# Kernel tuning notes

Hardware: AMD Instinct MI355X
Metric: run time of the kernel (lower is better)

The kernel has to match this reference:

```python
import jax, jax.numpy as jnp
import numpy as np

L, H, M, KB = 8, 512, 32, 256  # layers, hidden, fourier modes, key bits
EPS = 1e-5


def setup_inputs() -> dict:
    key = jax.random.key(0)
    ks = jax.random.split(key, 20)
    B, S = 8, 2048
    s = 0.02
    return {
        'x': jax.random.normal(ks[0], (B, S), jnp.float32),
        # input projection Linear(1, H): weight [H] (squeezed), bias [H]
        'in_w': jax.random.normal(ks[1], (H,), jnp.float32) * s,
        'in_b': jax.random.normal(ks[2], (H,), jnp.float32) * s,
        # per-layer fourier weights (complex, stored as real/imag), conv1d(k=1), layernorm
        'fw_r': jax.random.normal(ks[3], (L, M, H, H), jnp.float32) * s,
        'fw_i': jax.random.normal(ks[4], (L, M, H, H), jnp.float32) * s,
        'conv_w': jax.random.normal(ks[5], (L, H, H), jnp.float32) / np.sqrt(H),
        'conv_b': jax.random.normal(ks[6], (L, H), jnp.float32) * s,
        'ln_g': jnp.ones((L, H), jnp.float32),
        'ln_b': jnp.zeros((L, H), jnp.float32),
        # output projection H -> H/2 -> H/4 -> 1
        'op1_w': jax.random.normal(ks[7], (H // 2, H), jnp.float32) / np.sqrt(H),
        'op1_b': jnp.zeros((H // 2,), jnp.float32),
        'op2_w': jax.random.normal(ks[8], (H // 4, H // 2), jnp.float32) / np.sqrt(H // 2),
        'op2_b': jnp.zeros((H // 4,), jnp.float32),
        'op3_w': jax.random.normal(ks[9], (1, H // 4), jnp.float32) / np.sqrt(H // 4),
        'op3_b': jnp.zeros((1,), jnp.float32),
        # cryptanalytic head H -> H -> KB (sigmoid)
        'h1_w': jax.random.normal(ks[10], (H, H), jnp.float32) / np.sqrt(H),
        'h1_b': jnp.zeros((H,), jnp.float32),
        'h2_w': jax.random.normal(ks[11], (KB, H), jnp.float32) / np.sqrt(H),
        'h2_b': jnp.zeros((KB,), jnp.float32),
    }


def _gelu(x):
    return jax.nn.gelu(x, approximate=False)


def _fourier_layer(x, Wc, cw, cb, g, b):
    # x: [B, S, H]; Wc: [M, H, H] complex
    S = x.shape[1]
    x_ft = jnp.fft.rfft(x, axis=1)  # [B, F, H] complex, F = S//2+1
    m = min(M, x_ft.shape[1])
    # batched per-mode complex GEMM (replaces python loop over modes)
    spec = jnp.einsum('bmh,mhk->bmk', x_ft[:, :m], Wc[:m])
    out_ft = jnp.concatenate([spec, jnp.zeros_like(x_ft[:, m:])], axis=1)
    x_fourier = jnp.fft.irfft(out_ft, n=S, axis=1)  # real [B, S, H]
    x_conv = x @ cw.T + cb  # Conv1d kernel-size-1 == per-position linear
    y = x_fourier + x_conv
    mu = jnp.mean(y, axis=-1, keepdims=True)
    var = jnp.var(y, axis=-1, keepdims=True)
    return (y - mu) * jax.lax.rsqrt(var + EPS) * g + b


def reference(x, in_w, in_b, fw_r, fw_i, conv_w, conv_b, ln_g, ln_b,
              op1_w, op1_b, op2_w, op2_b, op3_w, op3_b,
              h1_w, h1_b, h2_w, h2_b):
    # input projection: Linear(1, H) on x[..., None]
    h = x[:, :, None] * in_w[None, None, :] + in_b  # [B, S, H]
    Wc = fw_r + 1j * fw_i  # [L, M, H, H]
    for l in range(L):
        h = _fourier_layer(h, Wc[l], conv_w[l], conv_b[l], ln_g[l], ln_b[l]) + h
    # output projection (dropout is identity in eval)
    o = _gelu(h @ op1_w.T + op1_b)
    o = _gelu(o @ op2_w.T + op2_b)
    output = (o @ op3_w.T + op3_b)[..., 0]  # [B, S]
    gf = jnp.mean(h, axis=1)  # [B, H]
    k = _gelu(gf @ h1_w.T + h1_b)
    key_pred = jax.nn.sigmoid(k @ h2_w.T + h2_b)  # [B, KB]
    return output, key_pred
```

## Files before the change

kernel.cpp:

```cpp
#include <hip/hip_runtime.h>
#include <hip/hip_bf16.h>
#include <math.h>

#define BB   8
#define SEQ  2048
#define HD   512
#define LAY  8
#define MD   32
#define NKB  256
#define LNEPS 1e-5f

typedef __attribute__((ext_vector_type(8))) short v8s;
typedef __attribute__((ext_vector_type(4))) float v4f;
typedef __attribute__((ext_vector_type(4))) unsigned short v4us;

__device__ __forceinline__ float b2f(__hip_bfloat16 v) { return __bfloat162float(v); }
__device__ __forceinline__ float geluf(float v) { return v * 0.5f * (1.f + erff(v * 0.70710678118654752f)); }
__device__ __forceinline__ float bflo(unsigned int u) { return __uint_as_float((u & 0xFFFFu) << 16); }
__device__ __forceinline__ float bfhi(unsigned int u) { return __uint_as_float(u & 0xFFFF0000u); }

__device__ __forceinline__ float ldin(const void* p, size_t i, int bf) {
    if (bf) return __bfloat162float(((const __hip_bfloat16*)p)[i]);
    return ((const float*)p)[i];
}
__device__ __forceinline__ void stout(void* p, size_t i, float v, int bf) {
    if (bf) ((__hip_bfloat16*)p)[i] = __float2bfloat16(v);
    else    ((float*)p)[i] = v;
}

__device__ __forceinline__ void gl2lds16(const void* g, void* l) {
    __builtin_amdgcn_global_load_lds((__attribute__((address_space(1))) void*)g,
                                     (__attribute__((address_space(3))) void*)l, 16, 0, 0);
}

__device__ __forceinline__ unsigned short f2bfu(float f) {
    __hip_bfloat16 b = __float2bfloat16(f);
    return *(unsigned short*)&b;
}

__global__ void k_flag(const unsigned int* __restrict__ lng_bits, int* __restrict__ flag) {
    if (threadIdx.x == 0 && blockIdx.x == 0)
        *flag = (lng_bits[0] == 0x3F803F80u) ? 1 : 0;
}

__global__ void k_setup(const void* __restrict__ x, const void* __restrict__ in_w, const void* __restrict__ in_b,
                        const void* __restrict__ cw, const void* __restrict__ w1, const void* __restrict__ w2,
                        const void* __restrict__ h1w, const void* __restrict__ h2w,
                        __hip_bfloat16* __restrict__ Ffwd, __hip_bfloat16* __restrict__ T2,
                        __hip_bfloat16* __restrict__ cwbf, __hip_bfloat16* __restrict__ w1bf,
                        __hip_bfloat16* __restrict__ w2bf, float* __restrict__ h1T, float* __restrict__ h2T,
                        float* __restrict__ h,
                        float* __restrict__ gf,
                        const int* __restrict__ flag) {
    int bf = *flag;
    int blk = blockIdx.x, t = threadIdx.x;
    if (blk < 512) {
        int idx = blk * 256 + t;
        int j = idx >> 11, s = idx & 2047;
        int m = j >> 1;
        int phase = (m * s) & (SEQ - 1);
        float ang = (float)phase * (6.283185307179586f / (float)SEQ);
        Ffwd[idx] = __float2bfloat16((j & 1) ? -sinf(ang) : cosf(ang));
    } else if (blk < 1024) {
        int idx = (blk - 512) * 256 + t;
        int s = idx >> 6, j = idx & 63;
        int m = j >> 1;
        float v;
        if (j == 0)      v = 1.f / (float)SEQ;
        else if (j == 1) v = 0.f;
        else {
            int phase = (m * s) & (SEQ - 1);
            float ang = (float)phase * (6.283185307179586f / (float)SEQ);
            v = (j & 1) ? (-2.f / (float)SEQ) * sinf(ang) : (2.f / (float)SEQ) * cosf(ang);
        }
        T2[idx] = __float2bfloat16(v);
    } else if (blk < 9216) {
        int idx = (blk - 1024) * 256 + t;
        cwbf[idx] = __float2bfloat16(ldin(cw, idx, bf));
    } else if (blk < 9728) {
        int idx = (blk - 9216) * 256 + t;
        w1bf[idx] = __float2bfloat16(ldin(w1, idx, bf));
    } else if (blk < 9856) {
        int idx = (blk - 9728) * 256 + t;
        w2bf[idx] = __float2bfloat16(ldin(w2, idx, bf));
    } else if (blk < 10880) {
        int idx = (blk - 9856) * 256 + t;
        int r = idx & 511, c = idx >> 9;
        h1T[idx] = ldin(h1w, (size_t)r * 512 + c, bf);
    } else if (blk < 11392) {
        int idx = (blk - 10880) * 256 + t;
        int r = idx & 255, c = idx >> 8;
        h2T[idx] = ldin(h2w, (size_t)r * 512 + c, bf);
    } else if (blk < 11408) {
        int idx = (blk - 11392) * 256 + t;
        gf[idx] = 0.f;
    } else {
        int idx = (blk - 11408) * 256 + t;
        int j = idx & 511;
        int bs = idx >> 9;
        float v = ldin(x, bs, bf) * ldin(in_w, j, bf) + ldin(in_b, j, bf);
        h[idx] = v;
    }
}

__global__ __launch_bounds__(256) void k_fdft2(const float* __restrict__ h,
                                               const __hip_bfloat16* __restrict__ Ffwd,
                                               float* __restrict__ Xpart) {
    __shared__ __align__(16) __hip_bfloat16 Als[2][16 * 72];
    int t = threadIdx.x;
    int lane = t & 63, wv = t >> 6;
    int ln15 = lane & 15, quad = lane >> 4;
    int ht = blockIdx.x, b = blockIdx.y, kh = blockIdx.z;
    int kcs = kh * 16;
    int sr = t >> 2, hc = (t & 3) * 4;

    v4f acc = (v4f){0.f, 0.f, 0.f, 0.f};

    const float* asrc0 = h + (size_t)b * SEQ * HD + ht * 16;
    const __hip_bfloat16* fbase = Ffwd + (size_t)(wv * 16 + ln15) * SEQ + quad * 8;

    float4 cur = *(const float4*)(asrc0 + (size_t)(kcs * 64 + sr) * HD + hc);
    {
        const float* cf = (const float*)&cur;
#pragma unroll
        for (int e = 0; e < 4; e++)
            Als[0][(hc + e) * 72 + sr] = __float2bfloat16(cf[e]);
    }
    __syncthreads();
    for (int i = 0; i < 16; i++) {
        int buf = i & 1;
        float4 nxt = cur;
        if (i < 15)
            nxt = *(const float4*)(asrc0 + (size_t)((kcs + i + 1) * 64 + sr) * HD + hc);
        v8s bf0 = *(const v8s*)(fbase + (kcs + i) * 64);
        v8s bf1 = *(const v8s*)(fbase + (kcs + i) * 64 + 32);
        v8s af0 = *(const v8s*)&Als[buf][ln15 * 72 + quad * 8];
        v8s af1 = *(const v8s*)&Als[buf][ln15 * 72 + 32 + quad * 8];
        acc = __builtin_amdgcn_mfma_f32_16x16x32_bf16(af0, bf0, acc, 0, 0, 0);
        acc = __builtin_amdgcn_mfma_f32_16x16x32_bf16(af1, bf1, acc, 0, 0, 0);
        if (i < 15) {
            const float* nf = (const float*)&nxt;
#pragma unroll
            for (int e = 0; e < 4; e++)
                Als[buf ^ 1][(hc + e) * 72 + sr] = __float2bfloat16(nf[e]);
        }
        __syncthreads();
        cur = nxt;
    }
    int j = wv * 16 + ln15;
    int m = j >> 1, c = j & 1;
    int hg = ht * 16 + quad * 4;
    float* outp = Xpart + (size_t)kh * 262144 + (size_t)(b * 32 + m) * 1024;
#pragma unroll
    for (int r = 0; r < 4; r++)
        outp[(size_t)(hg + r) * 2 + c] = acc[r];
}

__global__ __launch_bounds__(512) void k_mixp(const float* __restrict__ Xp0, const float* __restrict__ Xp1,
                                              const void* __restrict__ fwr, const void* __restrict__ fwi,
                                              float* __restrict__ Ppart, int l,
                                              const int* __restrict__ flag) {
    int bf = *flag;
    int ht = blockIdx.x;
    int m  = blockIdx.y;
    int t  = threadIdx.x;
    __shared__ float xs[8192];
    for (int e = t; e < 8192; e += 512) {
        int bb = e >> 10, r = e & 1023;
        size_t off = (size_t)(bb * 32 + m) * 1024 + r;
        xs[e] = Xp0[off] + Xp1[off];
    }
    __syncthreads();
    float ar[8], ai[8];
#pragma unroll
    for (int bb = 0; bb < 8; bb++) { ar[bb] = 0.f; ai[bb] = 0.f; }
    size_t wbase = (size_t)(l * 32 + m) * 262144;
    const float2* xs2 = (const float2*)xs;
    int h0 = ht * 32;
    if (bf) {
        const __hip_bfloat16* fr = (const __hip_bfloat16*)fwr;
        const __hip_bfloat16* fi = (const __hip_bfloat16*)fwi;
#pragma unroll 4
        for (int hh = h0; hh < h0 + 32; hh++) {
            float wr = b2f(fr[wbase + (size_t)hh * 512 + t]);
            float wi = b2f(fi[wbase + (size_t)hh * 512 + t]);
#pragma unroll
            for (int bb = 0; bb < 8; bb++) {
                float2 x2 = xs2[bb * 512 + hh];
                ar[bb] += x2.x * wr - x2.y * wi;
                ai[bb] += x2.x * wi + x2.y * wr;
            }
        }
    } else {
        const float* fr = (const float*)fwr;
        const float* fi = (const float*)fwi;
#pragma unroll 4
        for (int hh = h0; hh < h0 + 32; hh++) {
            float wr = fr[wbase + (size_t)hh * 512 + t];
            float wi = fi[wbase + (size_t)hh * 512 + t];
#pragma unroll
            for (int bb = 0; bb < 8; bb++) {
                float2 x2 = xs2[bb * 512 + hh];
                ar[bb] += x2.x * wr - x2.y * wi;
                ai[bb] += x2.x * wi + x2.y * wr;
            }
        }
    }
    float2* pp = (float2*)Ppart;
#pragma unroll
    for (int bb = 0; bb < 8; bb++)
        pp[((size_t)(m * 16 + ht) * 8 + bb) * 512 + t] = (float2){ar[bb], ai[bb]};
}

__global__ __launch_bounds__(256) void k_mixr(const float* __restrict__ Ppart,
                                              __hip_bfloat16* __restrict__ spec2) {
    int g = blockIdx.x * 256 + threadIdx.x;
    int k = g & 511, b = (g >> 9) & 7, m = g >> 12;
    const float2* pp = (const float2*)Ppart;
    float sr = 0.f, si = 0.f;
#pragma unroll
    for (int ht = 0; ht < 16; ht++) {
        float2 v = pp[((size_t)(m * 16 + ht) * 8 + b) * 512 + k];
        sr += v.x; si += v.y;
    }
    size_t o = ((size_t)(b * 512 + k) << 6) + 2 * m;
    __hip_bfloat16 hr = __float2bfloat16(sr), hi = __float2bfloat16(si);
    unsigned int pk = (unsigned int)*(unsigned short*)&hr | ((unsigned int)*(unsigned short*)&hi << 16);
    *(unsigned int*)(spec2 + o) = pk;
}

__global__ __launch_bounds__(512) void k_gln(__hip_bfloat16* __restrict__ hbf,
                                             const __hip_bfloat16* __restrict__ cwbf,
                                             const __hip_bfloat16* __restrict__ T2,
                                             const __hip_bfloat16* __restrict__ spec2,
                                             const void* __restrict__ cb,
                                             const void* __restrict__ lng, const void* __restrict__ lnb,
                                             float* __restrict__ h,
                                             int l, const int* __restrict__ flag) {
    int bfv = *flag;
    __shared__ __align__(16) __hip_bfloat16 smem[2][19456];
    __shared__ float stats[128];
    __hip_bfloat16* Yls = &smem[0][0];

    int t = threadIdx.x;
    int lane = t & 63, wv = t >> 6;
    int wr = wv >> 2, wc = wv & 3;
    int ln15 = lane & 15, quad = lane >> 4;
    int row0 = blockIdx.x * 64;
    int b = row0 >> 11, s0 = row0 & 2047;
    int arow = t >> 3, acolq = (t & 7) * 4;

    v4f acc[16];
#pragma unroll
    for (int i = 0; i < 16; i++) acc[i] = (v4f){0.f, 0.f, 0.f, 0.f};

    const __hip_bfloat16* cwl = cwbf + (size_t)l * 262144;

    auto stageB = [&](int buf, int kc) {
        int k0 = kc * 32;
#pragma unroll
        for (int p = 0; p < 4; p++) {
            int i = p * 512 + t;
            int n = i >> 2, kq = (i & 3) * 8;
            const __hip_bfloat16* bsrc = (k0 < 512)
                ? cwl + (size_t)n * 512 + k0 + kq
                : spec2 + (size_t)(b * 512 + n) * 64 + (k0 - 512) + kq;
            gl2lds16(bsrc, &smem[buf][2560 + (size_t)(p * 512 + wv * 64) * 8]);
        }
    };
    auto loadA = [&](int kc, float4& av, v4us& tv) {
        int k0 = kc * 32;
        if (k0 < 512) {
            av = *(const float4*)&h[(size_t)(row0 + arow) * HD + k0 + acolq];
        } else {
            tv = *(const v4us*)&T2[(size_t)(s0 + arow) * 64 + (k0 - 512) + acolq];
        }
    };
    auto writeA = [&](int buf, int kc, const float4& av, const v4us& tv) {
        __hip_bfloat16* dst = &smem[buf][arow * 40 + acolq];
        if (kc * 32 < 512) {
            const float* af = (const float*)&av;
            v4us pk;
#pragma unroll
            for (int e = 0; e < 4; e++) pk[e] = (short)f2bfu(af[e]);
            *(v4us*)dst = pk;
        } else {
            *(v4us*)dst = tv;
        }
    };

    {
        float4 av; v4us tv;
        loadA(0, av, tv);
        stageB(0, 0);
        writeA(0, 0, av, tv);
    }
    __syncthreads();
    int cur = 0;
    float4 avn; v4us tvn;
    for (int kc = 0; kc < 18; kc++) {
        if (kc < 17) {
            loadA(kc + 1, avn, tvn);
            stageB(cur ^ 1, kc + 1);
        }
        const __hip_bfloat16* Als = &smem[cur][0];
        const __hip_bfloat16* Bls = &smem[cur][2560];
        v8s af[2], bfr[8];
#pragma unroll
        for (int i = 0; i < 2; i++)
            af[i] = *(const v8s*)&Als[(wr * 32 + i * 16 + ln15) * 40 + quad * 8];
#pragma unroll
        for (int j = 0; j < 8; j++)
            bfr[j] = *(const v8s*)&Bls[(wc * 128 + j * 16 + ln15) * 32 + quad * 8];
#pragma unroll
        for (int i = 0; i < 2; i++)
#pragma unroll
            for (int j = 0; j < 8; j++)
                acc[i * 8 + j] = __builtin_amdgcn_mfma_f32_16x16x32_bf16(af[i], bfr[j], acc[i * 8 + j], 0, 0, 0);
        if (kc < 17) writeA(cur ^ 1, kc + 1, avn, tvn);
        __syncthreads();
        cur ^= 1;
    }
#pragma unroll
    for (int j = 0; j < 8; j++) {
        int col = wc * 128 + j * 16 + ln15;
        float cbv = ldin(cb, l * HD + col, bfv);
#pragma unroll
        for (int i = 0; i < 2; i++) {
            int rl = wr * 32 + i * 16 + quad * 4;
#pragma unroll
            for (int r = 0; r < 4; r++)
                Yls[(rl + r) * 520 + col] = __float2bfloat16(acc[i * 8 + j][r] + cbv);
        }
    }
    __syncthreads();
    {
        int r = t >> 3, g2 = t & 7;
        float s = 0.f, q = 0.f;
        for (int i = 0; i < 32; i++) {
            int cp = g2 + i * 8;
            unsigned int u = *(const unsigned int*)&Yls[r * 520 + cp * 2];
            float v0 = bflo(u), v1 = bfhi(u);
            s += v0 + v1; q += v0 * v0 + v1 * v1;
        }
        s += __shfl_xor(s, 1); s += __shfl_xor(s, 2); s += __shfl_xor(s, 4);
        q += __shfl_xor(q, 1); q += __shfl_xor(q, 2); q += __shfl_xor(q, 4);
        if (g2 == 0) {
            float mu = s * (1.f / (float)HD);
            float var = q * (1.f / (float)HD) - mu * mu;
            stats[r * 2] = mu; stats[r * 2 + 1] = rsqrtf(var + LNEPS);
        }
    }
    __syncthreads();
    {
        int c2 = t & 255;
        int gc = 2 * c2;
        float g0 = ldin(lng, l * HD + gc, bfv),     g1 = ldin(lng, l * HD + gc + 1, bfv);
        float b0 = ldin(lnb, l * HD + gc, bfv),     b1 = ldin(lnb, l * HD + gc + 1, bfv);
        int rbase = t >> 8;
        int last = (l == LAY - 1);
        for (int k = 0; k < 32; k++) {
            int r = rbase + 2 * k;
            float mu = stats[r * 2], rs = stats[r * 2 + 1];
            unsigned int u = *(const unsigned int*)&Yls[r * 520 + c2 * 2];
            float v0 = bflo(u), v1 = bfhi(u);
            float2 hv = *(const float2*)&h[(size_t)(row0 + r) * HD + gc];
            float n0 = (v0 - mu) * rs * g0 + b0 + hv.x;
            float n1 = (v1 - mu) * rs * g1 + b1 + hv.y;
            *(float2*)&h[(size_t)(row0 + r) * HD + gc] = (float2){n0, n1};
            if (last) {
                unsigned int up = ((unsigned int)f2bfu(n1) << 16) | (unsigned int)f2bfu(n0);
                ((unsigned int*)(hbf + (size_t)(row0 + r) * HD))[c2] = up;
            }
        }
    }
}

__global__ __launch_bounds__(256) void k_pj1(const __hip_bfloat16* __restrict__ hbf,
                                             const __hip_bfloat16* __restrict__ w1bf,
                                             const void* __restrict__ b1,
                                             __hip_bfloat16* __restrict__ o1bf,
                                             const int* __restrict__ flag) {
    int bfv = *flag;
    __shared__ __align__(16) __hip_bfloat16 smem[2][8192];
    int t = threadIdx.x;
    int lane = t & 63, wv = t >> 6;
    int wr = wv >> 1, wc = wv & 1;
    int ln15 = lane & 15, quad = lane >> 4;
    int row0 = blockIdx.x * 128, n0 = blockIdx.y * 128;

    v4f acc[16];
#pragma unroll
    for (int i = 0; i < 16; i++) acc[i] = (v4f){0.f, 0.f, 0.f, 0.f};

    auto stage = [&](int buf, int kc) {
        int k0 = kc * 32;
#pragma unroll
        for (int p = 0; p < 2; p++) {
            int i = p * 256 + t;
            int row = i >> 2, kq = (i & 3) * 8;
            gl2lds16(hbf + (size_t)(row0 + row) * 512 + k0 + kq, &smem[buf][(size_t)(p * 256 + wv * 64) * 8]);
            gl2lds16(w1bf + (size_t)(n0 + row) * 512 + k0 + kq, &smem[buf][4096 + (size_t)(p * 256 + wv * 64) * 8]);
        }
    };

    stage(0, 0);
    __syncthreads();
    int cur = 0;
    for (int kc = 0; kc < 16; kc++) {
        if (kc < 15) stage(cur ^ 1, kc + 1);
        const __hip_bfloat16* Als = &smem[cur][0];
        const __hip_bfloat16* Bls = &smem[cur][4096];
        v8s af[4], bfr[4];
#pragma unroll
        for (int i = 0; i < 4; i++)
            af[i] = *(const v8s*)&Als[(wr * 64 + i * 16 + ln15) * 32 + quad * 8];
#pragma unroll
        for (int j = 0; j < 4; j++)
            bfr[j] = *(const v8s*)&Bls[(wc * 64 + j * 16 + ln15) * 32 + quad * 8];
#pragma unroll
        for (int i = 0; i < 4; i++)
#pragma unroll
            for (int j = 0; j < 4; j++)
                acc[i * 4 + j] = __builtin_amdgcn_mfma_f32_16x16x32_bf16(af[i], bfr[j], acc[i * 4 + j], 0, 0, 0);
        __syncthreads();
        cur ^= 1;
    }
#pragma unroll
    for (int j = 0; j < 4; j++) {
        int col = n0 + wc * 64 + j * 16 + ln15;
        float bv = ldin(b1, col, bfv);
#pragma unroll
        for (int i = 0; i < 4; i++) {
            int rg = row0 + wr * 64 + i * 16 + quad * 4;
#pragma unroll
            for (int r = 0; r < 4; r++)
                o1bf[(size_t)(rg + r) * 256 + col] = __float2bfloat16(geluf(acc[i * 4 + j][r] + bv));
        }
    }
}

__global__ __launch_bounds__(256) void k_pj2(const __hip_bfloat16* __restrict__ o1bf,
                                             const __hip_bfloat16* __restrict__ w2bf,
                                             const void* __restrict__ b2,
                                             const void* __restrict__ w3, const void* __restrict__ b3,
                                             void* __restrict__ out, const int* __restrict__ flag) {
    int bfv = *flag;
    __shared__ __align__(16) __hip_bfloat16 smem[2][8192];
    __shared__ __hip_bfloat16 o2s[128 * 130];
    __shared__ float w3s[128];
    int t = threadIdx.x;
    int lane = t & 63, wv = t >> 6;
    int wr = wv >> 1, wc = wv & 1;
    int ln15 = lane & 15, quad = lane >> 4;
    int row0 = blockIdx.x * 128;
    if (t < 128) w3s[t] = ldin(w3, t, bfv);

    v4f acc[16];
#pragma unroll
    for (int i = 0; i < 16; i++) acc[i] = (v4f){0.f, 0.f, 0.f, 0.f};

    auto stage = [&](int buf, int kc) {
        int k0 = kc * 32;
#pragma unroll
        for (int p = 0; p < 2; p++) {
            int i = p * 256 + t;
            int row = i >> 2, kq = (i & 3) * 8;
            gl2lds16(o1bf + (size_t)(row0 + row) * 256 + k0 + kq, &smem[buf][(size_t)(p * 256 + wv * 64) * 8]);
            gl2lds16(w2bf + (size_t)row * 256 + k0 + kq,          &smem[buf][4096 + (size_t)(p * 256 + wv * 64) * 8]);
        }
    };

    stage(0, 0);
    __syncthreads();
    int cur = 0;
    for (int kc = 0; kc < 8; kc++) {
        if (kc < 7) stage(cur ^ 1, kc + 1);
        const __hip_bfloat16* Als = &smem[cur][0];
        const __hip_bfloat16* Bls = &smem[cur][4096];
        v8s af[4], bfr[4];
#pragma unroll
        for (int i = 0; i < 4; i++)
            af[i] = *(const v8s*)&Als[(wr * 64 + i * 16 + ln15) * 32 + quad * 8];
#pragma unroll
        for (int j = 0; j < 4; j++)
            bfr[j] = *(const v8s*)&Bls[(wc * 64 + j * 16 + ln15) * 32 + quad * 8];
#pragma unroll
        for (int i = 0; i < 4; i++)
#pragma unroll
            for (int j = 0; j < 4; j++)
                acc[i * 4 + j] = __builtin_amdgcn_mfma_f32_16x16x32_bf16(af[i], bfr[j], acc[i * 4 + j], 0, 0, 0);
        __syncthreads();
        cur ^= 1;
    }
#pragma unroll
    for (int j = 0; j < 4; j++) {
        int col = wc * 64 + j * 16 + ln15;
        float bv = ldin(b2, col, bfv);
#pragma unroll
        for (int i = 0; i < 4; i++) {
            int rl = wr * 64 + i * 16 + quad * 4;
#pragma unroll
            for (int r = 0; r < 4; r++)
                o2s[(rl + r) * 130 + col] = __float2bfloat16(geluf(acc[i * 4 + j][r] + bv));
        }
    }
    __syncthreads();
    if (t < 128) {
        float s = 0.f;
        for (int j = 0; j < 128; j++) s += b2f(o2s[t * 130 + j]) * w3s[j];
        stout(out, row0 + t, s + ldin(b3, 0, bfv), bfv);
    }
}

__global__ __launch_bounds__(512) void k_gf(const float* __restrict__ h, float* __restrict__ gf) {
    int sc = blockIdx.x, b = blockIdx.y;
    int j = threadIdx.x;
    const float* p = h + ((size_t)b * SEQ + sc * 64) * HD + j;
    float s = 0.f;
    for (int i = 0; i < 64; i++) s += p[(size_t)i * HD];
    atomicAdd(&gf[b * HD + j], s * (1.f / (float)SEQ));
}

__global__ __launch_bounds__(512) void k_head(const float* __restrict__ gf,
                                              const float* __restrict__ h1T, const void* __restrict__ h1b,
                                              const float* __restrict__ h2T, const void* __restrict__ h2b,
                                              void* __restrict__ out, const int* __restrict__ flag) {
    int bf = *flag;
    int b = blockIdx.x;
    int t = threadIdx.x;
    __shared__ float gs[512];
    __shared__ float ks[512];
    gs[t] = gf[b * HD + t];
    __syncthreads();
    float a = 0.f;
    for (int j = 0; j < 512; j++) a += gs[j] * h1T[j * 512 + t];
    ks[t] = geluf(a + ldin(h1b, t, bf));
    __syncthreads();
    if (t < 256) {
        float s = 0.f;
        for (int j = 0; j < 512; j++) s += ks[j] * h2T[j * 256 + t];
        s += ldin(h2b, t, bf);
        stout(out, BB * SEQ + b * NKB + t, 1.f / (1.f + expf(-s)), bf);
    }
}

extern "C" void kernel_launch(void* const* d_in, const int* in_sizes, int n_in,
                              void* d_out, int out_size, void* d_ws, size_t ws_size,
                              hipStream_t stream) {
    const void* x    = d_in[0];
    const void* in_w = d_in[1];
    const void* in_b = d_in[2];
    const void* fwr  = d_in[3];
    const void* fwi  = d_in[4];
    const void* cw   = d_in[5];
    const void* cb   = d_in[6];
    const void* lng  = d_in[7];
    const void* lnb  = d_in[8];
    const void* w1   = d_in[9];
    const void* b1   = d_in[10];
    const void* w2   = d_in[11];
    const void* b2   = d_in[12];
    const void* w3   = d_in[13];
    const void* b3   = d_in[14];
    const void* h1w  = d_in[15];
    const void* h1b  = d_in[16];
    const void* h2w  = d_in[17];
    const void* h2b  = d_in[18];

    float* ws = (float*)d_ws;
    __hip_bfloat16* Ffwd = (__hip_bfloat16*)ws;
    float*          h    = ws + 131072;
    float*          Xp   = h + 8388608;
    __hip_bfloat16* o1bf = (__hip_bfloat16*)Xp;
    __hip_bfloat16* hbf  = (__hip_bfloat16*)(Xp + 4194304);
    __hip_bfloat16* cwbf = (__hip_bfloat16*)(Xp + 8388608);
    __hip_bfloat16* T2   = (__hip_bfloat16*)(Xp + 10485760);
    __hip_bfloat16* spec2= (__hip_bfloat16*)(Xp + 10551296);
    float*          XftOld = Xp + 10682368;
    float*          gf   = XftOld + 262144;
    float*          w1T  = gf + 4096;
    __hip_bfloat16* w1bf = (__hip_bfloat16*)w1T;
    __hip_bfloat16* w2bf = (__hip_bfloat16*)(w1T + 65536);
    float*          w2T  = w1T + 131072;
    float*          h1T  = w2T + 32768;
    float*          h2T  = h1T + 262144;
    int*            flag = (int*)(h2T + 131072);
    float*          Xpart = h2T + 131072 + 64;
    float*          Ppart = Xpart + 524288;

    k_flag<<<1, 1, 0, stream>>>((const unsigned int*)lng, flag);
    k_setup<<<44176, 256, 0, stream>>>(x, in_w, in_b, cw, w1, w2, h1w, h2w,
                                       Ffwd, T2, cwbf, w1bf, w2bf, h1T, h2T,
                                       h, gf, flag);

    for (int l = 0; l < LAY; l++) {
        k_fdft2<<<dim3(32, 8, 2), 256, 0, stream>>>(h, Ffwd, Xpart);
        k_mixp<<<dim3(16, 32), 512, 0, stream>>>(Xpart, Xpart + 262144, fwr, fwi, Ppart, l, flag);
        k_mixr<<<512, 256, 0, stream>>>(Ppart, spec2);
        k_gln<<<256, 512, 0, stream>>>(hbf, cwbf, T2, spec2, cb, lng, lnb, h, l, flag);
    }

    k_gf<<<dim3(32, 8), 512, 0, stream>>>(h, gf);
    k_pj1<<<dim3(128, 2), 256, 0, stream>>>(hbf, w1bf, b1, o1bf, flag);
    k_pj2<<<128, 256, 0, stream>>>(o1bf, w2bf, b2, w3, b3, d_out, flag);
    k_head<<<8, 512, 0, stream>>>(gf, h1T, h1b, h2T, h2b, d_out, flag);
}
```

Baseline: 1.140 ms.

## Halve k_gln row tile to 32 and fuse sequence-mean into last layer

The fused conv+spectral GEMM/LayerNorm kernel now processes 32 rows per block instead of 64, doubling the grid to 512 blocks so more CUs are busy. Each wave computes one 16-row MFMA tile instead of two. The separate k_gf mean-pooling kernel is removed and its work is done with per-block atomic adds in the final layer. The trade-off is that every B tile (conv weights and spectral data) is reloaded twice as often, and each B load now feeds half as much MFMA work.

```diff
diff --git a/kernel.cpp b/kernel.cpp
--- a/kernel.cpp
+++ b/kernel.cpp
@@ -235,24 +235,24 @@
                                              const __hip_bfloat16* __restrict__ spec2,
                                              const void* __restrict__ cb,
                                              const void* __restrict__ lng, const void* __restrict__ lnb,
-                                             float* __restrict__ h,
+                                             float* __restrict__ h, float* __restrict__ gf,
                                              int l, const int* __restrict__ flag) {
     int bfv = *flag;
-    __shared__ __align__(16) __hip_bfloat16 smem[2][19456];
-    __shared__ float stats[128];
+    __shared__ __align__(16) __hip_bfloat16 smem[2][17920];
+    __shared__ float stats[64];
     __hip_bfloat16* Yls = &smem[0][0];
 
     int t = threadIdx.x;
     int lane = t & 63, wv = t >> 6;
     int wr = wv >> 2, wc = wv & 3;
     int ln15 = lane & 15, quad = lane >> 4;
-    int row0 = blockIdx.x * 64;
+    int row0 = blockIdx.x * 32;
     int b = row0 >> 11, s0 = row0 & 2047;
-    int arow = t >> 3, acolq = (t & 7) * 4;
-
-    v4f acc[16];
-#pragma unroll
-    for (int i = 0; i < 16; i++) acc[i] = (v4f){0.f, 0.f, 0.f, 0.f};
+    int arow = t >> 4, acol2 = (t & 15) * 2;
+
+    v4f acc[8];
+#pragma unroll
+    for (int i = 0; i < 8; i++) acc[i] = (v4f){0.f, 0.f, 0.f, 0.f};
 
     const __hip_bfloat16* cwl = cwbf + (size_t)l * 262144;
 
@@ -265,58 +265,50 @@
             const __hip_bfloat16* bsrc = (k0 < 512)
                 ? cwl + (size_t)n * 512 + k0 + kq
                 : spec2 + (size_t)(b * 512 + n) * 64 + (k0 - 512) + kq;
-            gl2lds16(bsrc, &smem[buf][2560 + (size_t)(p * 512 + wv * 64) * 8]);
+            gl2lds16(bsrc, &smem[buf][1280 + (size_t)(p * 512 + wv * 64) * 8]);
         }
     };
-    auto loadA = [&](int kc, float4& av, v4us& tv) {
+    auto loadA = [&](int kc, float2& av, unsigned int& tv) {
         int k0 = kc * 32;
         if (k0 < 512) {
-            av = *(const float4*)&h[(size_t)(row0 + arow) * HD + k0 + acolq];
+            av = *(const float2*)&h[(size_t)(row0 + arow) * HD + k0 + acol2];
         } else {
-            tv = *(const v4us*)&T2[(size_t)(s0 + arow) * 64 + (k0 - 512) + acolq];
+            tv = *(const unsigned int*)&T2[(size_t)(s0 + arow) * 64 + (k0 - 512) + acol2];
         }
     };
-    auto writeA = [&](int buf, int kc, const float4& av, const v4us& tv) {
-        __hip_bfloat16* dst = &smem[buf][arow * 40 + acolq];
+    auto writeA = [&](int buf, int kc, const float2& av, unsigned int tv) {
+        unsigned int* dst = (unsigned int*)&smem[buf][arow * 40 + acol2];
         if (kc * 32 < 512) {
-            const float* af = (const float*)&av;
-            v4us pk;
-#pragma unroll
-            for (int e = 0; e < 4; e++) pk[e] = (short)f2bfu(af[e]);
-            *(v4us*)dst = pk;
+            *dst = (unsigned int)f2bfu(av.x) | ((unsigned int)f2bfu(av.y) << 16);
         } else {
-            *(v4us*)dst = tv;
+            *dst = tv;
         }
     };
 
     {
-        float4 av; v4us tv;
+        float2 av; unsigned int tv;
         loadA(0, av, tv);
         stageB(0, 0);
         writeA(0, 0, av, tv);
     }
     __syncthreads();
     int cur = 0;
-    float4 avn; v4us tvn;
+    float2 avn; unsigned int tvn;
     for (int kc = 0; kc < 18; kc++) {
         if (kc < 17) {
             loadA(kc + 1, avn, tvn);
             stageB(cur ^ 1, kc + 1);
         }
         const __hip_bfloat16* Als = &smem[cur][0];
-        const __hip_bfloat16* Bls = &smem[cur][2560];
-        v8s af[2], bfr[8];
-#pragma unroll
-        for (int i = 0; i < 2; i++)
-            af[i] = *(const v8s*)&Als[(wr * 32 + i * 16 + ln15) * 40 + quad * 8];
+        const __hip_bfloat16* Bls = &smem[cur][1280];
+        v8s af = *(const v8s*)&Als[(wr * 16 + ln15) * 40 + quad * 8];
+        v8s bfr[8];
 #pragma unroll
         for (int j = 0; j < 8; j++)
             bfr[j] = *(const v8s*)&Bls[(wc * 128 + j * 16 + ln15) * 32 + quad * 8];
 #pragma unroll
-        for (int i = 0; i < 2; i++)
-#pragma unroll
-            for (int j = 0; j < 8; j++)
-                acc[i * 8 + j] = __builtin_amdgcn_mfma_f32_16x16x32_bf16(af[i], bfr[j], acc[i * 8 + j], 0, 0, 0);
+        for (int j = 0; j < 8; j++)
+            acc[j] = __builtin_amdgcn_mfma_f32_16x16x32_bf16(af, bfr[j], acc[j], 0, 0, 0);
         if (kc < 17) writeA(cur ^ 1, kc + 1, avn, tvn);
         __syncthreads();
         cur ^= 1;
@@ -325,26 +317,23 @@
     for (int j = 0; j < 8; j++) {
         int col = wc * 128 + j * 16 + ln15;
         float cbv = ldin(cb, l * HD + col, bfv);
-#pragma unroll
-        for (int i = 0; i < 2; i++) {
-            int rl = wr * 32 + i * 16 + quad * 4;
-#pragma unroll
-            for (int r = 0; r < 4; r++)
-                Yls[(rl + r) * 520 + col] = __float2bfloat16(acc[i * 8 + j][r] + cbv);
-        }
+        int rl = wr * 16 + quad * 4;
+#pragma unroll
+        for (int r = 0; r < 4; r++)
+            Yls[(rl + r) * 520 + col] = __float2bfloat16(acc[j][r] + cbv);
     }
     __syncthreads();
     {
-        int r = t >> 3, g2 = t & 7;
+        int r = t >> 4, g2 = t & 15;
         float s = 0.f, q = 0.f;
-        for (int i = 0; i < 32; i++) {
-            int cp = g2 + i * 8;
+        for (int i = 0; i < 16; i++) {
+            int cp = g2 + i * 16;
             unsigned int u = *(const unsigned int*)&Yls[r * 520 + cp * 2];
             float v0 = bflo(u), v1 = bfhi(u);
             s += v0 + v1; q += v0 * v0 + v1 * v1;
         }
-        s += __shfl_xor(s, 1); s += __shfl_xor(s, 2); s += __shfl_xor(s, 4);
-        q += __shfl_xor(q, 1); q += __shfl_xor(q, 2); q += __shfl_xor(q, 4);
+        s += __shfl_xor(s, 1); s += __shfl_xor(s, 2); s += __shfl_xor(s, 4); s += __shfl_xor(s, 8);
+        q += __shfl_xor(q, 1); q += __shfl_xor(q, 2); q += __shfl_xor(q, 4); q += __shfl_xor(q, 8);
         if (g2 == 0) {
             float mu = s * (1.f / (float)HD);
             float var = q * (1.f / (float)HD) - mu * mu;
@@ -359,7 +348,8 @@
         float b0 = ldin(lnb, l * HD + gc, bfv),     b1 = ldin(lnb, l * HD + gc + 1, bfv);
         int rbase = t >> 8;
         int last = (l == LAY - 1);
-        for (int k = 0; k < 32; k++) {
+        float gs0 = 0.f, gs1 = 0.f;
+        for (int k = 0; k < 16; k++) {
             int r = rbase + 2 * k;
             float mu = stats[r * 2], rs = stats[r * 2 + 1];
             unsigned int u = *(const unsigned int*)&Yls[r * 520 + c2 * 2];
@@ -371,7 +361,12 @@
             if (last) {
                 unsigned int up = ((unsigned int)f2bfu(n1) << 16) | (unsigned int)f2bfu(n0);
                 ((unsigned int*)(hbf + (size_t)(row0 + r) * HD))[c2] = up;
+                gs0 += n0; gs1 += n1;
             }
+        }
+        if (last) {
+            atomicAdd(&gf[b * HD + gc],     gs0 * (1.f / (float)SEQ));
+            atomicAdd(&gf[b * HD + gc + 1], gs1 * (1.f / (float)SEQ));
         }
     }
 }
@@ -511,15 +506,6 @@
         for (int j = 0; j < 128; j++) s += b2f(o2s[t * 130 + j]) * w3s[j];
         stout(out, row0 + t, s + ldin(b3, 0, bfv), bfv);
     }
-}
-
-__global__ __launch_bounds__(512) void k_gf(const float* __restrict__ h, float* __restrict__ gf) {
-    int sc = blockIdx.x, b = blockIdx.y;
-    int j = threadIdx.x;
-    const float* p = h + ((size_t)b * SEQ + sc * 64) * HD + j;
-    float s = 0.f;
-    for (int i = 0; i < 64; i++) s += p[(size_t)i * HD];
-    atomicAdd(&gf[b * HD + j], s * (1.f / (float)SEQ));
 }
 
 __global__ __launch_bounds__(512) void k_head(const float* __restrict__ gf,
@@ -598,10 +584,9 @@
         k_fdft2<<<dim3(32, 8, 2), 256, 0, stream>>>(h, Ffwd, Xpart);
         k_mixp<<<dim3(16, 32), 512, 0, stream>>>(Xpart, Xpart + 262144, fwr, fwi, Ppart, l, flag);
         k_mixr<<<512, 256, 0, stream>>>(Ppart, spec2);
-        k_gln<<<256, 512, 0, stream>>>(hbf, cwbf, T2, spec2, cb, lng, lnb, h, l, flag);
-    }
-
-    k_gf<<<dim3(32, 8), 512, 0, stream>>>(h, gf);
+        k_gln<<<512, 512, 0, stream>>>(hbf, cwbf, T2, spec2, cb, lng, lnb, h, gf, l, flag);
+    }
+
     k_pj1<<<dim3(128, 2), 256, 0, stream>>>(hbf, w1bf, b1, o1bf, flag);
     k_pj2<<<128, 256, 0, stream>>>(o1bf, w2bf, b2, w3, b3, d_out, flag);
     k_head<<<8, 512, 0, stream>>>(gf, h1T, h1b, h2T, h2b, d_out, flag);
```

Result: slower. 1.174 ms (+2.9%).
